# Performance work log

Measured on AMD Instinct MI355X. Metric: run time of the kernel, lower is better.

Reference implementation:

```python
import jax, jax.numpy as jnp
import numpy as np

B, T, IN, H = 32, 512, 1024, 1024


def setup_inputs() -> dict:
    key = jax.random.key(0)
    k1, k2, k3, k4, k5 = jax.random.split(key, 5)
    std = 1.0 / np.sqrt(H)
    return {
        "inputs": jax.random.normal(k1, (B, T, IN), dtype=jnp.float32),
        "h0": jnp.zeros((1, B, H), dtype=jnp.float32),
        "c0": jnp.zeros((1, B, H), dtype=jnp.float32),
        "W_ih": jax.random.uniform(k2, (4 * H, IN), dtype=jnp.float32, minval=-std, maxval=std),
        "b_ih": jax.random.uniform(k3, (4 * H,), dtype=jnp.float32, minval=-std, maxval=std),
        "W_hh": jax.random.uniform(k4, (4 * H, H), dtype=jnp.float32, minval=-std, maxval=std),
        "b_hh": jax.random.uniform(k5, (4 * H,), dtype=jnp.float32, minval=-std, maxval=std),
    }


def reference(inputs, h0, c0, W_ih, b_ih, W_hh, b_hh):
    Hd = W_hh.shape[1]
    # Precompute input projection for all timesteps at once: [B, T, 4H]
    x_proj = jnp.einsum('bti,gi->btg', inputs, W_ih) + b_ih
    xs = jnp.swapaxes(x_proj, 0, 1)  # [T, B, 4H]

    def step(carry, x_t):
        h, c = carry  # [B, H] each
        preact = x_t + h @ W_hh.T + b_hh  # [B, 4H]
        gates = jax.nn.sigmoid(preact[:, :3 * Hd])
        g_t = jnp.tanh(preact[:, 3 * Hd:])
        i_t = gates[:, :Hd]
        f_t = gates[:, Hd:2 * Hd]
        o_t = gates[:, 2 * Hd:]
        c_t = c * f_t + i_t * g_t
        h_t = o_t * jnp.tanh(c_t)
        return (h_t, c_t), h_t

    (h_f, c_f), hs = jax.lax.scan(step, (h0[0], c0[0]), xs)
    logits = jnp.swapaxes(hs, 0, 1)  # [B, T, H]
    return logits, h_f[None], c_f[None]
```

## Files before the change

kernel.cpp:

```cpp
#include <hip/hip_runtime.h>
#include <hip/hip_cooperative_groups.h>

namespace cg = cooperative_groups;

constexpr int Bb = 32;
constexpr int Tt = 512;
constexpr int KI = 1024;
constexpr int HH = 1024;


__device__ __forceinline__ void st_sys(float* p, float v) {
    __hip_atomic_store(p, v, __ATOMIC_RELAXED, __HIP_MEMORY_SCOPE_SYSTEM);
}
__device__ __forceinline__ unsigned long long ld_sys64(const unsigned long long* p) {
    return __hip_atomic_load(p, __ATOMIC_RELAXED, __HIP_MEMORY_SCOPE_SYSTEM);
}

__global__ void prep_kernel(const float4* __restrict__ in4,
                            const float* __restrict__ h0,
                            float4* __restrict__ xT4,
                            float4* __restrict__ hbuf4,
                            unsigned* bar)
{
    int idx = blockIdx.x * 256 + threadIdx.x;
    if (idx == 0) __hip_atomic_store(bar, 0u, __ATOMIC_RELAXED, __HIP_MEMORY_SCOPE_SYSTEM);
    constexpr int NX = Bb * Tt * (KI / 4);
    if (idx < NX) {
        int kq = idx & 255;
        int t  = (idx >> 8) & 511;
        int b  = idx >> 17;
        xT4[((size_t)t * 256 + kq) * 32 + b] = in4[idx];
    } else {
        int r = idx - NX;
        if (r < (HH / 4) * Bb) {
            int b  = r & 31;
            int jq = r >> 5;
            hbuf4[(size_t)jq * 32 + b] = *(const float4*)(h0 + (size_t)b * HH + jq * 4);
        }
    }
}

__global__ void logits_kernel(const float4* __restrict__ hbuf4, float4* __restrict__ out4)
{
    int idx = blockIdx.x * 256 + threadIdx.x;
    constexpr int N = Bb * Tt * (HH / 4);
    if (idx >= N) return;
    int j4 = idx & 255;
    int t  = (idx >> 8) & 511;
    int b  = idx >> 17;
    out4[idx] = hbuf4[((size_t)(t + 1) * 256 + j4) * 32 + b];
}

template<int STRIDE>
__device__ __forceinline__ void dot32(const float4* __restrict__ xp,
                                      const float4* const* __restrict__ wr,
                                      float4 acc[8])
{
#pragma unroll 4
    for (int i = 0; i < 32; ++i) {
        float4 xv = xp[(size_t)i * STRIDE];
#pragma unroll
        for (int r = 0; r < 8; ++r) {
            float4 wv = wr[r][i];
            acc[r].x = fmaf(wv.x, xv.x, acc[r].x);
            acc[r].y = fmaf(wv.y, xv.y, acc[r].y);
            acc[r].z = fmaf(wv.z, xv.z, acc[r].z);
            acc[r].w = fmaf(wv.w, xv.w, acc[r].w);
        }
    }
}

__device__ __forceinline__ void dot32_sys(const float* __restrict__ hp,
                                          const float4* const* __restrict__ wr,
                                          float4 acc[8])
{
#pragma unroll 8
    for (int i = 0; i < 32; ++i) {
        const unsigned long long* q = (const unsigned long long*)(hp + (size_t)i * 128);
        unsigned long long lo = ld_sys64(q);
        unsigned long long hi = ld_sys64(q + 1);
        float hx = __uint_as_float((unsigned)(lo & 0xffffffffull));
        float hy = __uint_as_float((unsigned)(lo >> 32));
        float hz = __uint_as_float((unsigned)(hi & 0xffffffffull));
        float hw = __uint_as_float((unsigned)(hi >> 32));
#pragma unroll
        for (int r = 0; r < 8; ++r) {
            float4 wv = wr[r][i];
            acc[r].x = fmaf(wv.x, hx, acc[r].x);
            acc[r].y = fmaf(wv.y, hy, acc[r].y);
            acc[r].z = fmaf(wv.z, hz, acc[r].z);
            acc[r].w = fmaf(wv.w, hw, acc[r].w);
        }
    }
}

template<bool GATHER>
__global__ __launch_bounds__(512, 2)
void lstm_seq(const float* __restrict__ inputs,
              const float* __restrict__ h0,
              const float* __restrict__ c0,
              const float* __restrict__ W_ih,
              const float* __restrict__ b_ih,
              const float* __restrict__ W_hh,
              const float* __restrict__ b_hh,
              const float4* __restrict__ xT4,
              float4* __restrict__ hbuf4,
              unsigned* bar,
              float* __restrict__ out)
{
    cg::grid_group grid = cg::this_grid();
    const int tid  = threadIdx.x;
    const int bid  = blockIdx.x;
    const int w    = tid >> 6;
    const int lane = tid & 63;
    const int b    = lane & 31;
    const int half = lane >> 5;
    const int j0   = bid * 4;

    const float4* wx[8];
    const float4* wh[8];
#pragma unroll
    for (int r = 0; r < 8; ++r) {
        int rr  = half * 8 + r;
        int row = (rr & 3) * HH + j0 + (rr >> 2);
        wx[r] = (const float4*)(W_ih + (size_t)row * KI) + w * 32;
        wh[r] = (const float4*)(W_hh + (size_t)row * HH) + w * 32;
    }

    __shared__ float part[16][8][33];

    const int cb = tid >> 2;
    const int cj = tid & 3;
    float c_reg = 0.f;
    float bsum[4] = {0.f, 0.f, 0.f, 0.f};
    if (tid < 128) {
        c_reg = c0[(size_t)cb * HH + j0 + cj];
#pragma unroll
        for (int g = 0; g < 4; ++g) {
            int row = g * HH + j0 + cj;
            bsum[g] = b_ih[row] + b_hh[row];
        }
    }

    float* logits = out;
    float* h_f = out + (size_t)Bb * Tt * HH;
    float* c_f = h_f + (size_t)Bb * HH;

    float4 xacc[8];
#pragma unroll
    for (int r = 0; r < 8; ++r) xacc[r] = make_float4(0.f, 0.f, 0.f, 0.f);
    if (!GATHER) {
        dot32<32>(xT4 + (size_t)0 * 8192 + w * 1024 + b, wx, xacc);
    } else {
        dot32<1>((const float4*)(inputs + ((size_t)b * Tt + 0) * KI) + w * 32, wx, xacc);
    }

    for (int t = 0; t < Tt; ++t) {
        float4 hacc[8];
#pragma unroll
        for (int r = 0; r < 8; ++r) hacc[r] = make_float4(0.f, 0.f, 0.f, 0.f);
        if (!GATHER) {
            dot32_sys((const float*)(hbuf4 + (size_t)t * 8192 + w * 1024 + b), wh, hacc);
        } else {
            const float4* hp = (t == 0)
                ? (const float4*)(h0 + (size_t)b * HH) + w * 32
                : (const float4*)(logits + ((size_t)b * Tt + (t - 1)) * HH) + w * 32;
            dot32<1>(hp, wh, hacc);
        }

#pragma unroll
        for (int r = 0; r < 8; ++r) {
            float s = (hacc[r].x + hacc[r].y) + (hacc[r].z + hacc[r].w)
                    + (xacc[r].x + xacc[r].y) + (xacc[r].z + xacc[r].w);
            part[half * 8 + r][w][b] = s;
        }
        __syncthreads();

        if (tid < 128) {
            float pr[4];
#pragma unroll
            for (int g = 0; g < 4; ++g) {
                float s = bsum[g];
#pragma unroll
                for (int ww = 0; ww < 8; ++ww) s += part[cj * 4 + g][ww][cb];
                pr[g] = s;
            }
            float ig = 1.f / (1.f + expf(-pr[0]));
            float fg = 1.f / (1.f + expf(-pr[1]));
            float og = 1.f / (1.f + expf(-pr[2]));
            float gg = tanhf(pr[3]);
            c_reg = c_reg * fg + ig * gg;
            float hv = og * tanhf(c_reg);
            if (!GATHER) {
                st_sys((float*)hbuf4 + ((size_t)(t + 1) * 256 + bid) * 128 + tid, hv);
            } else {
                logits[((size_t)cb * Tt + t) * HH + j0 + cj] = hv;
            }
            if (t == Tt - 1) h_f[(size_t)cb * HH + j0 + cj] = hv;
        }

        if (!GATHER) {
            asm volatile("s_waitcnt vmcnt(0)" ::: "memory");
            __syncthreads();
            if (tid == 0) {
                __hip_atomic_fetch_add(bar, 1u, __ATOMIC_RELAXED, __HIP_MEMORY_SCOPE_SYSTEM);
            }
            if (t + 1 < Tt) {
#pragma unroll
                for (int r = 0; r < 8; ++r) xacc[r] = make_float4(0.f, 0.f, 0.f, 0.f);
                dot32<32>(xT4 + (size_t)(t + 1) * 8192 + w * 1024 + b, wx, xacc);
            }
            if (tid == 0) {
                unsigned target = (unsigned)(t + 1) * (unsigned)gridDim.x;
                while (__hip_atomic_load(bar, __ATOMIC_RELAXED, __HIP_MEMORY_SCOPE_SYSTEM) < target) {
                    __builtin_amdgcn_s_sleep(2);
                }
            }
            __syncthreads();
        } else {
            if (t + 1 < Tt) {
#pragma unroll
                for (int r = 0; r < 8; ++r) xacc[r] = make_float4(0.f, 0.f, 0.f, 0.f);
                dot32<1>((const float4*)(inputs + ((size_t)b * Tt + (t + 1)) * KI) + w * 32, wx, xacc);
            }
            if (tid < 128) __threadfence();
            grid.sync();
        }
    }
    if (tid < 128) c_f[(size_t)cb * HH + j0 + cj] = c_reg;
}

extern "C" void kernel_launch(void* const* d_in, const int* in_sizes, int n_in,
                              void* d_out, int out_size, void* d_ws, size_t ws_size,
                              hipStream_t stream)
{
    const float* inputs = (const float*)d_in[0];
    const float* h0     = (const float*)d_in[1];
    const float* c0     = (const float*)d_in[2];
    const float* W_ih   = (const float*)d_in[3];
    const float* b_ih   = (const float*)d_in[4];
    const float* W_hh   = (const float*)d_in[5];
    const float* b_hh   = (const float*)d_in[6];
    float* out = (float*)d_out;

    float4* xT4   = (float4*)d_ws;
    float4* hbuf4 = xT4 + (size_t)Tt * (KI / 4) * Bb;
    unsigned* bar = (unsigned*)(hbuf4 + (size_t)(Tt + 1) * (HH / 4) * Bb);
    const size_t need = ((size_t)Tt * (KI / 4) * Bb + (size_t)(Tt + 1) * (HH / 4) * Bb) * sizeof(float4) + 64;

    const float4* xT4c = xT4;

    if (ws_size >= need) {
        prep_kernel<<<dim3(16416), dim3(256), 0, stream>>>((const float4*)inputs, h0, xT4, hbuf4, bar);
        void (*k)(const float*, const float*, const float*, const float*, const float*,
                  const float*, const float*, const float4*, float4*, unsigned*, float*) = lstm_seq<false>;
        void* args[] = { (void*)&inputs, (void*)&h0, (void*)&c0, (void*)&W_ih, (void*)&b_ih,
                         (void*)&W_hh, (void*)&b_hh, (void*)&xT4c, (void*)&hbuf4, (void*)&bar, (void*)&out };
        hipLaunchCooperativeKernel((const void*)k, dim3(256), dim3(512), args, 0, stream);
        logits_kernel<<<dim3(16384), dim3(256), 0, stream>>>(hbuf4, (float4*)out);
    } else {
        void (*k)(const float*, const float*, const float*, const float*, const float*,
                  const float*, const float*, const float4*, float4*, unsigned*, float*) = lstm_seq<true>;
        void* args[] = { (void*)&inputs, (void*)&h0, (void*)&c0, (void*)&W_ih, (void*)&b_ih,
                         (void*)&W_hh, (void*)&b_hh, (void*)&xT4c, (void*)&hbuf4, (void*)&bar, (void*)&out };
        hipLaunchCooperativeKernel((const void*)k, dim3(256), dim3(512), args, 0, stream);
    }
}
```

Before: 19.14 ms.

## Replace atomic counter grid barrier with per-block flags and agent-scope atomics

Each block now publishes its completed step number to its own padded flag slot instead of incrementing one shared counter. A full wavefront polls all 256 flags in parallel and exits when every flag has reached the target. The h-state loads, stores and flags also move from system scope to agent scope. The aim is to remove contention on a single atomic and the extra cost of system-coherent memory traffic on the per-step barrier, at the cost of more polling loads per block.

```diff
diff --git a/kernel.cpp b/kernel.cpp
--- a/kernel.cpp
+++ b/kernel.cpp
@@ -9,21 +9,26 @@
 constexpr int HH = 1024;
 
 
-__device__ __forceinline__ void st_sys(float* p, float v) {
-    __hip_atomic_store(p, v, __ATOMIC_RELAXED, __HIP_MEMORY_SCOPE_SYSTEM);
-}
-__device__ __forceinline__ unsigned long long ld_sys64(const unsigned long long* p) {
-    return __hip_atomic_load(p, __ATOMIC_RELAXED, __HIP_MEMORY_SCOPE_SYSTEM);
+__device__ __forceinline__ void st_agent(float* p, float v) {
+    __hip_atomic_store(p, v, __ATOMIC_RELAXED, __HIP_MEMORY_SCOPE_AGENT);
+}
+__device__ __forceinline__ unsigned long long ld_agent64(const unsigned long long* p) {
+    return __hip_atomic_load(p, __ATOMIC_RELAXED, __HIP_MEMORY_SCOPE_AGENT);
+}
+__device__ __forceinline__ void st_flag(unsigned* p, unsigned v) {
+    __hip_atomic_store(p, v, __ATOMIC_RELAXED, __HIP_MEMORY_SCOPE_AGENT);
+}
+__device__ __forceinline__ unsigned ld_flag(const unsigned* p) {
+    return __hip_atomic_load(p, __ATOMIC_RELAXED, __HIP_MEMORY_SCOPE_AGENT);
 }
 
 __global__ void prep_kernel(const float4* __restrict__ in4,
                             const float* __restrict__ h0,
                             float4* __restrict__ xT4,
                             float4* __restrict__ hbuf4,
-                            unsigned* bar)
+                            unsigned* __restrict__ flags)
 {
     int idx = blockIdx.x * 256 + threadIdx.x;
-    if (idx == 0) __hip_atomic_store(bar, 0u, __ATOMIC_RELAXED, __HIP_MEMORY_SCOPE_SYSTEM);
     constexpr int NX = Bb * Tt * (KI / 4);
     if (idx < NX) {
         int kq = idx & 255;
@@ -36,6 +41,8 @@
             int b  = r & 31;
             int jq = r >> 5;
             hbuf4[(size_t)jq * 32 + b] = *(const float4*)(h0 + (size_t)b * HH + jq * 4);
+        } else if (r < (HH / 4) * Bb + 256) {
+            flags[(r - (HH / 4) * Bb) * 16] = 0u;
         }
     }
 }
@@ -70,15 +77,15 @@
     }
 }
 
-__device__ __forceinline__ void dot32_sys(const float* __restrict__ hp,
-                                          const float4* const* __restrict__ wr,
-                                          float4 acc[8])
+__device__ __forceinline__ void dot32_agent(const float* __restrict__ hp,
+                                            const float4* const* __restrict__ wr,
+                                            float4 acc[8])
 {
 #pragma unroll 8
     for (int i = 0; i < 32; ++i) {
         const unsigned long long* q = (const unsigned long long*)(hp + (size_t)i * 128);
-        unsigned long long lo = ld_sys64(q);
-        unsigned long long hi = ld_sys64(q + 1);
+        unsigned long long lo = ld_agent64(q);
+        unsigned long long hi = ld_agent64(q + 1);
         float hx = __uint_as_float((unsigned)(lo & 0xffffffffull));
         float hy = __uint_as_float((unsigned)(lo >> 32));
         float hz = __uint_as_float((unsigned)(hi & 0xffffffffull));
@@ -105,7 +112,7 @@
               const float* __restrict__ b_hh,
               const float4* __restrict__ xT4,
               float4* __restrict__ hbuf4,
-              unsigned* bar,
+              unsigned* __restrict__ flags,
               float* __restrict__ out)
 {
     cg::grid_group grid = cg::this_grid();
@@ -160,7 +167,7 @@
 #pragma unroll
         for (int r = 0; r < 8; ++r) hacc[r] = make_float4(0.f, 0.f, 0.f, 0.f);
         if (!GATHER) {
-            dot32_sys((const float*)(hbuf4 + (size_t)t * 8192 + w * 1024 + b), wh, hacc);
+            dot32_agent((const float*)(hbuf4 + (size_t)t * 8192 + w * 1024 + b), wh, hacc);
         } else {
             const float4* hp = (t == 0)
                 ? (const float4*)(h0 + (size_t)b * HH) + w * 32
@@ -192,7 +199,7 @@
             c_reg = c_reg * fg + ig * gg;
             float hv = og * tanhf(c_reg);
             if (!GATHER) {
-                st_sys((float*)hbuf4 + ((size_t)(t + 1) * 256 + bid) * 128 + tid, hv);
+                st_agent((float*)hbuf4 + ((size_t)(t + 1) * 256 + bid) * 128 + tid, hv);
             } else {
                 logits[((size_t)cb * Tt + t) * HH + j0 + cj] = hv;
             }
@@ -203,17 +210,23 @@
             asm volatile("s_waitcnt vmcnt(0)" ::: "memory");
             __syncthreads();
             if (tid == 0) {
-                __hip_atomic_fetch_add(bar, 1u, __ATOMIC_RELAXED, __HIP_MEMORY_SCOPE_SYSTEM);
+                st_flag(flags + bid * 16, (unsigned)(t + 1));
             }
             if (t + 1 < Tt) {
 #pragma unroll
                 for (int r = 0; r < 8; ++r) xacc[r] = make_float4(0.f, 0.f, 0.f, 0.f);
                 dot32<32>(xT4 + (size_t)(t + 1) * 8192 + w * 1024 + b, wx, xacc);
             }
-            if (tid == 0) {
-                unsigned target = (unsigned)(t + 1) * (unsigned)gridDim.x;
-                while (__hip_atomic_load(bar, __ATOMIC_RELAXED, __HIP_MEMORY_SCOPE_SYSTEM) < target) {
-                    __builtin_amdgcn_s_sleep(2);
+            if (tid < 64) {
+                const unsigned target = (unsigned)(t + 1);
+                for (;;) {
+                    unsigned m0 = ld_flag(flags + (tid * 4 + 0) * 16);
+                    unsigned m1 = ld_flag(flags + (tid * 4 + 1) * 16);
+                    unsigned m2 = ld_flag(flags + (tid * 4 + 2) * 16);
+                    unsigned m3 = ld_flag(flags + (tid * 4 + 3) * 16);
+                    bool ok = (m0 >= target) && (m1 >= target) && (m2 >= target) && (m3 >= target);
+                    if (__all(ok)) break;
+                    __builtin_amdgcn_s_sleep(1);
                 }
             }
             __syncthreads();
@@ -243,26 +256,27 @@
     const float* b_hh   = (const float*)d_in[6];
     float* out = (float*)d_out;
 
-    float4* xT4   = (float4*)d_ws;
-    float4* hbuf4 = xT4 + (size_t)Tt * (KI / 4) * Bb;
-    unsigned* bar = (unsigned*)(hbuf4 + (size_t)(Tt + 1) * (HH / 4) * Bb);
-    const size_t need = ((size_t)Tt * (KI / 4) * Bb + (size_t)(Tt + 1) * (HH / 4) * Bb) * sizeof(float4) + 64;
+    float4* xT4    = (float4*)d_ws;
+    float4* hbuf4  = xT4 + (size_t)Tt * (KI / 4) * Bb;
+    unsigned* flags = (unsigned*)(hbuf4 + (size_t)(Tt + 1) * (HH / 4) * Bb);
+    const size_t need = ((size_t)Tt * (KI / 4) * Bb + (size_t)(Tt + 1) * (HH / 4) * Bb) * sizeof(float4)
+                      + 256 * 16 * sizeof(unsigned);
 
     const float4* xT4c = xT4;
 
     if (ws_size >= need) {
-        prep_kernel<<<dim3(16416), dim3(256), 0, stream>>>((const float4*)inputs, h0, xT4, hbuf4, bar);
+        prep_kernel<<<dim3(16417), dim3(256), 0, stream>>>((const float4*)inputs, h0, xT4, hbuf4, flags);
         void (*k)(const float*, const float*, const float*, const float*, const float*,
                   const float*, const float*, const float4*, float4*, unsigned*, float*) = lstm_seq<false>;
         void* args[] = { (void*)&inputs, (void*)&h0, (void*)&c0, (void*)&W_ih, (void*)&b_ih,
-                         (void*)&W_hh, (void*)&b_hh, (void*)&xT4c, (void*)&hbuf4, (void*)&bar, (void*)&out };
+                         (void*)&W_hh, (void*)&b_hh, (void*)&xT4c, (void*)&hbuf4, (void*)&flags, (void*)&out };
         hipLaunchCooperativeKernel((const void*)k, dim3(256), dim3(512), args, 0, stream);
         logits_kernel<<<dim3(16384), dim3(256), 0, stream>>>(hbuf4, (float4*)out);
     } else {
         void (*k)(const float*, const float*, const float*, const float*, const float*,
                   const float*, const float*, const float4*, float4*, unsigned*, float*) = lstm_seq<true>;
         void* args[] = { (void*)&inputs, (void*)&h0, (void*)&c0, (void*)&W_ih, (void*)&b_ih,
-                         (void*)&W_hh, (void*)&b_hh, (void*)&xT4c, (void*)&hbuf4, (void*)&bar, (void*)&out };
+                         (void*)&W_hh, (void*)&b_hh, (void*)&xT4c, (void*)&hbuf4, (void*)&flags, (void*)&out };
         hipLaunchCooperativeKernel((const void*)k, dim3(256), dim3(512), args, 0, stream);
     }
 }
```

Measured after the change: 19.16 ms. About the same (+0.1%).
